# Kernel optimization log

Hardware: AMD Instinct MI355X
Metric: run time of the kernel (lower is better)

Reference implementation:

```python
import jax, jax.numpy as jnp
import numpy as np

G, N, E, F, C, H = 2, 20000, 160000, 128, 64, 8
NEG_SLOPE = 0.2


def setup_inputs() -> dict:
    key = jax.random.key(0)
    ks = jax.random.split(key, 16)
    def w(k, shape, fan_in):
        return jax.random.normal(k, shape, jnp.float32) * (1.0 / np.sqrt(fan_in))
    z = lambda *s: jnp.zeros(s, jnp.float32)
    return {
        "x": jax.random.normal(ks[0], (G, N, F), jnp.float32),
        "edge_index": jax.random.randint(ks[1], (G, 2, E), 0, N, jnp.int32),
        "edge_weight": jax.random.uniform(ks[2], (G, E), jnp.float32),
        "Wl1": w(ks[3], (F, H * C), F), "bl1": z(H * C),
        "Wr1": w(ks[4], (F, H * C), F), "br1": z(H * C),
        "We1": w(ks[5], (1, H * C), 1),
        "att1": w(ks[6], (H, C), C),
        "bias1": z(H * C),
        "Wl2": w(ks[7], (H * C, C), H * C), "bl2": z(C),
        "Wr2": w(ks[8], (H * C, C), H * C), "br2": z(C),
        "We2": w(ks[9], (1, C), 1),
        "att2": w(ks[10], (1, C), C),
        "bias2": z(C),
        "Wg": w(ks[11], (C, C), C), "bg": z(C),
        "Wn": w(ks[12], (2 * C, C), 2 * C), "bn": z(C),
        "Wo": w(ks[13], (C, 1), C), "bo": z(1),
    }


def _segment_softmax(logits, seg, n):
    m = jax.ops.segment_max(logits, seg, num_segments=n)
    ex = jnp.exp(logits - m[seg])
    den = jax.ops.segment_sum(ex, seg, num_segments=n)
    return ex / den[seg]


def _gatv2(x, src, dst, eattr, Wl, bl, Wr, br, We, att, bias, heads, concat):
    # Faithful PyG GATv2Conv (share_weights=False, edge_dim=1).
    n = x.shape[0]
    hc = Wl.shape[1]
    c = hc // heads
    xl = (x @ Wl + bl).reshape(n, heads, c)   # lin_l (source / message)
    xr = (x @ Wr + br).reshape(n, heads, c)   # lin_r (target)
    ee = (eattr @ We).reshape(-1, heads, c)   # lin_edge (bias=False)
    s = jax.nn.leaky_relu(xl[src] + xr[dst] + ee, NEG_SLOPE)  # [Etot, H, C]
    logit = jnp.einsum('ehc,hc->eh', s, att)
    alpha = _segment_softmax(logit, dst, n)   # softmax over incoming edges
    out = jax.ops.segment_sum(alpha[..., None] * xl[src], dst, num_segments=n)
    out = out.reshape(n, hc) if concat else out.mean(axis=1)
    return out + bias


def _forward(edge_index, x, edge_weight, Wl1, bl1, Wr1, br1, We1, att1, bias1,
             Wl2, bl2, Wr2, br2, We2, att2, bias2, Wg, bg, Wn, bn, Wo, bo):
    n = x.shape[1]
    def per_graph(xg, eig, ewg):
        src, dst = eig[0], eig[1]
        ea = ewg[:, None]  # edge_weight.unsqueeze(-1), edge_dim=1
        # add_self_loops with fill_value='mean' (mean of edge_attr grouped by dst)
        cnt = jax.ops.segment_sum(jnp.ones_like(ewg), dst, num_segments=n)
        loop = jax.ops.segment_sum(ea, dst, num_segments=n) / jnp.clip(cnt, 1.0)[:, None]
        ar = jnp.arange(n, dtype=src.dtype)
        src2 = jnp.concatenate([src, ar])
        dst2 = jnp.concatenate([dst, ar])
        ea2 = jnp.concatenate([ea, loop], axis=0)
        h = jax.nn.elu(_gatv2(xg, src2, dst2, ea2, Wl1, bl1, Wr1, br1, We1, att1, bias1, H, True))
        h = jax.nn.elu(_gatv2(h, src2, dst2, ea2, Wl2, bl2, Wr2, br2, We2, att2, bias2, 1, False))
        return h
    h = jax.vmap(per_graph)(x, edge_index, edge_weight)      # [G, N, C]
    g_emb = h.max(axis=1)                                    # global_max_pool per graph
    Gv = g_emb.max(axis=0)                                   # max over graphs -> [C]
    Gv = jax.nn.relu(Gv @ Wg + bg)
    Hc = jnp.concatenate([h, jnp.broadcast_to(Gv, h.shape)], axis=-1)  # [G,N,2C]
    h2 = jax.nn.relu(Hc @ Wn + bn)
    return (h2 @ Wo + bo)[..., 0]                            # [G, N] logits


def reference(x, edge_index, edge_weight, Wl1, bl1, Wr1, br1, We1, att1, bias1,
              Wl2, bl2, Wr2, br2, We2, att2, bias2, Wg, bg, Wn, bn, Wo, bo):
    return _forward(edge_index, x, edge_weight, Wl1, bl1, Wr1, br1, We1, att1, bias1,
                    Wl2, bl2, Wr2, br2, We2, att2, bias2, Wg, bg, Wn, bn, Wo, bo)
```

## Files before the change

### kernel.cpp

```cpp
#include <hip/hip_runtime.h>
#include <hip/hip_bf16.h>
#include <cstdint>
#include <cstddef>

#define NEG_SLOPE 0.2f

static constexpr int Gg = 2;
static constexpr int Nn = 20000;
static constexpr int Ee = 160000;
static constexpr int Ff = 128;
static constexpr int Cc = 64;
static constexpr int HC = 512;
static constexpr int GN = Gg * Nn;
static constexpr int GNP = 40064;

typedef __attribute__((ext_vector_type(8))) short short8;
typedef __attribute__((ext_vector_type(4))) float floatx4;

__device__ __forceinline__ float bf2f(unsigned short b) {
    return __uint_as_float(((unsigned)b) << 16);
}
__device__ __forceinline__ unsigned short f2bf(float x) {
    unsigned u = __float_as_uint(x);
    unsigned r = 0x7fffu + ((u >> 16) & 1u);
    return (unsigned short)((u + r) >> 16);
}
__device__ __forceinline__ void unpack8(const uint4 p, float* f) {
    f[0] = __uint_as_float(p.x << 16); f[1] = __uint_as_float(p.x & 0xffff0000u);
    f[2] = __uint_as_float(p.y << 16); f[3] = __uint_as_float(p.y & 0xffff0000u);
    f[4] = __uint_as_float(p.z << 16); f[5] = __uint_as_float(p.z & 0xffff0000u);
    f[6] = __uint_as_float(p.w << 16); f[7] = __uint_as_float(p.w & 0xffff0000u);
}
__device__ __forceinline__ unsigned encf(float x) {
    unsigned u = __float_as_uint(x);
    return (u & 0x80000000u) ? ~u : (u | 0x80000000u);
}
__device__ __forceinline__ float decf(unsigned e) {
    return __uint_as_float((e & 0x80000000u) ? (e ^ 0x80000000u) : ~e);
}

__global__ void zero_init_k(int* cnt, float* lsum, unsigned* gmax) {
    int idx = blockIdx.x * 256 + threadIdx.x;
    if (idx < GN) { cnt[idx] = 0; lsum[idx] = 0.f; }
    if (idx < 64) gmax[idx] = 0u;
}

__global__ void hist_k(const int* __restrict__ ei, const float* __restrict__ ew,
                       int* __restrict__ cnt, float* __restrict__ lsum) {
    int idx = blockIdx.x * 256 + threadIdx.x;
    if (idx >= Gg * Ee) return;
    int g = idx / Ee;
    int e = idx - g * Ee;
    int dst = ei[(size_t)g * 2 * Ee + Ee + e];
    float wv = ew[idx];
    atomicAdd(&cnt[g * Nn + dst], 1);
    atomicAdd(&lsum[g * Nn + dst], wv);
}

__global__ __launch_bounds__(1024) void scan_k(const int* __restrict__ cnt, const float* __restrict__ lsum,
                                               int* __restrict__ off, int* __restrict__ cur,
                                               float* __restrict__ loopw) {
    const int g = blockIdx.x;
    const int t = threadIdx.x;
    const int CH = 20;
    int base = t * CH;
    int cl[CH];
    int s = 0;
    if (base < Nn) {
#pragma unroll
        for (int q = 0; q < 5; ++q) {
            int4 v = *(const int4*)(cnt + (size_t)g * Nn + base + q * 4);
            cl[q * 4 + 0] = v.x; cl[q * 4 + 1] = v.y; cl[q * 4 + 2] = v.z; cl[q * 4 + 3] = v.w;
            s += v.x + v.y + v.z + v.w;
        }
    }
    __shared__ int sh[1024];
    sh[t] = s;
    __syncthreads();
    for (int d = 1; d < 1024; d <<= 1) {
        int v = (t >= d) ? sh[t - d] : 0;
        __syncthreads();
        sh[t] += v;
        __syncthreads();
    }
    int run = sh[t] - s;
    if (base < Nn) {
#pragma unroll
        for (int q = 0; q < 5; ++q) {
            int4 ov;
            ov.x = run; run += cl[q * 4 + 0];
            ov.y = run; run += cl[q * 4 + 1];
            ov.z = run; run += cl[q * 4 + 2];
            ov.w = run; run += cl[q * 4 + 3];
            *(int4*)(off + (size_t)g * Nn + base + q * 4) = ov;
            *(int4*)(cur + (size_t)g * Nn + base + q * 4) = ov;
            float4 lv = *(const float4*)(lsum + (size_t)g * Nn + base + q * 4);
            float4 lw;
            lw.x = lv.x / fmaxf((float)cl[q * 4 + 0], 1.f);
            lw.y = lv.y / fmaxf((float)cl[q * 4 + 1], 1.f);
            lw.z = lv.z / fmaxf((float)cl[q * 4 + 2], 1.f);
            lw.w = lv.w / fmaxf((float)cl[q * 4 + 3], 1.f);
            *(float4*)(loopw + (size_t)g * Nn + base + q * 4) = lw;
        }
    }
}

__global__ void scatter_k(const int* __restrict__ ei, const float* __restrict__ ew,
                          int* __restrict__ cur, int2* __restrict__ sedge) {
    int idx = blockIdx.x * 256 + threadIdx.x;
    if (idx >= Gg * Ee) return;
    int g = idx / Ee;
    int e = idx - g * Ee;
    int src = ei[(size_t)g * 2 * Ee + e];
    int dst = ei[(size_t)g * 2 * Ee + Ee + e];
    float wv = ew[idx];
    int pos = atomicAdd(&cur[g * Nn + dst], 1);
    int2 v; v.x = src; v.y = __float_as_int(wv);
    sedge[(size_t)g * Ee + pos] = v;
}

__global__ void castprep_k(const float* __restrict__ x, unsigned short* __restrict__ xb,
                           const float* __restrict__ Wl1, const float* __restrict__ Wr1,
                           const float* __restrict__ bl1, const float* __restrict__ br1,
                           const float* __restrict__ Wl2, const float* __restrict__ Wr2,
                           const float* __restrict__ bl2, const float* __restrict__ br2,
                           unsigned short* __restrict__ Wt1, unsigned short* __restrict__ Wt2,
                           float* __restrict__ b1cat, float* __restrict__ b2cat) {
    int t = blockIdx.x * 256 + threadIdx.x;
    size_t base = (size_t)t * 4;
    if (base < (size_t)GNP * Ff) {
        ushort4 ov;
        if (base < (size_t)GN * Ff) {
            float4 v = *(const float4*)(x + base);
            ov.x = f2bf(v.x); ov.y = f2bf(v.y); ov.z = f2bf(v.z); ov.w = f2bf(v.w);
        } else {
            ov.x = ov.y = ov.z = ov.w = 0;
        }
        *(ushort4*)(xb + base) = ov;
    }
    if (t < 1024 * 128) {
        int n = t >> 7, k = t & 127;
        float v = (n < 512) ? Wl1[(size_t)k * 512 + n] : Wr1[(size_t)k * 512 + n - 512];
        Wt1[t] = f2bf(v);
    }
    if (t < 128 * 512) {
        int n = t >> 9, k = t & 511;
        float v = (n < 64) ? Wl2[(size_t)k * 64 + n] : Wr2[(size_t)k * 64 + n - 64];
        Wt2[t] = f2bf(v);
    }
    if (t < 1024) b1cat[t] = (t < 512) ? bl1[t] : br1[t - 512];
    if (t < 128)  b2cat[t] = (t < 64) ? bl2[t] : br2[t - 64];
}

template <int K>
__global__ __launch_bounds__(256) void mfma_gemm_k(const unsigned short* __restrict__ A, int lda,
                                                   const unsigned short* __restrict__ Bt,
                                                   const float* __restrict__ bias,
                                                   unsigned short* __restrict__ Cg, int ldc,
                                                   int Mreal) {
    __shared__ unsigned short As[128 * 32];
    __shared__ unsigned short Bs[128 * 32];
    const int t = threadIdx.x;
    const int lane = t & 63;
    const int wid = t >> 6;
    const int wm = wid >> 1, wn = wid & 1;
    const int m0 = blockIdx.x * 128;
    const int n0 = blockIdx.y * 128;

    floatx4 acc[4][4] = {};

    const int jrow = t >> 2;
    const int js = t & 3;
    const int wavebase = (t & 192) * 16;

    for (int k0 = 0; k0 < K; k0 += 32) {
#pragma unroll
        for (int r = 0; r < 2; ++r) {
            int row = jrow + r * 64;
            int c = js ^ ((row >> 1) & 3);
            const unsigned short* gA = A + (size_t)(m0 + row) * lda + k0 + c * 8;
            const unsigned short* gB = Bt + (size_t)(n0 + row) * K + k0 + c * 8;
            __builtin_amdgcn_global_load_lds(
                (const __attribute__((address_space(1))) void*)gA,
                (__attribute__((address_space(3))) void*)((char*)As + r * 4096 + wavebase),
                16, 0, 0);
            __builtin_amdgcn_global_load_lds(
                (const __attribute__((address_space(1))) void*)gB,
                (__attribute__((address_space(3))) void*)((char*)Bs + r * 4096 + wavebase),
                16, 0, 0);
        }
        __syncthreads();

        const int lrow = lane & 15, lc = lane >> 4;
        short8 af[4], bf[4];
#pragma unroll
        for (int i2 = 0; i2 < 4; ++i2) {
            int rA = wm * 64 + i2 * 16 + lrow;
            int sA = lc ^ ((rA >> 1) & 3);
            af[i2] = *(const short8*)((const char*)As + (rA * 4 + sA) * 16);
        }
#pragma unroll
        for (int j2 = 0; j2 < 4; ++j2) {
            int rB = wn * 64 + j2 * 16 + lrow;
            int sB = lc ^ ((rB >> 1) & 3);
            bf[j2] = *(const short8*)((const char*)Bs + (rB * 4 + sB) * 16);
        }
#pragma unroll
        for (int i2 = 0; i2 < 4; ++i2)
#pragma unroll
            for (int j2 = 0; j2 < 4; ++j2)
                acc[i2][j2] = __builtin_amdgcn_mfma_f32_16x16x32_bf16(bf[j2], af[i2], acc[i2][j2], 0, 0, 0);
        __syncthreads();
    }

    const int mrow = m0 + wm * 64 + (lane & 15);
    const int ncol0 = n0 + wn * 64 + ((lane >> 4) << 2);
    float4 bq[4];
#pragma unroll
    for (int j2 = 0; j2 < 4; ++j2) bq[j2] = *(const float4*)(bias + ncol0 + j2 * 16);
#pragma unroll
    for (int i2 = 0; i2 < 4; ++i2) {
        int m = mrow + i2 * 16;
        if (m < Mreal) {
#pragma unroll
            for (int j2 = 0; j2 < 4; ++j2) {
                ushort4 ov;
                ov.x = f2bf(acc[i2][j2][0] + bq[j2].x);
                ov.y = f2bf(acc[i2][j2][1] + bq[j2].y);
                ov.z = f2bf(acc[i2][j2][2] + bq[j2].z);
                ov.w = f2bf(acc[i2][j2][3] + bq[j2].w);
                *(ushort4*)(Cg + (size_t)m * ldc + ncol0 + j2 * 16) = ov;
            }
        }
    }
}

__global__ __launch_bounds__(256) void agg1_k(const unsigned short* xlr,
                                              const int2* __restrict__ sedge,
                                              const int* __restrict__ off, const int* __restrict__ cnt,
                                              const float* __restrict__ loopw,
                                              const float* __restrict__ att1, const float* __restrict__ We1,
                                              const float* __restrict__ bias1,
                                              unsigned short* h1) {
    const int lane = threadIdx.x & 63;
    const int wid = (blockIdx.x << 2) + (threadIdx.x >> 6);
    if (wid >= GN) return;
    const int g = (wid >= Nn) ? 1 : 0;

    float attv[8], wev[8];
    {
        float4 a0 = *(const float4*)(att1 + lane * 8);
        float4 a1 = *(const float4*)(att1 + lane * 8 + 4);
        attv[0] = a0.x; attv[1] = a0.y; attv[2] = a0.z; attv[3] = a0.w;
        attv[4] = a1.x; attv[5] = a1.y; attv[6] = a1.z; attv[7] = a1.w;
        float4 w0 = *(const float4*)(We1 + lane * 8);
        float4 w1 = *(const float4*)(We1 + lane * 8 + 4);
        wev[0] = w0.x; wev[1] = w0.y; wev[2] = w0.z; wev[3] = w0.w;
        wev[4] = w1.x; wev[5] = w1.y; wev[6] = w1.z; wev[7] = w1.w;
    }
    float xrv[8];
    unpack8(((const uint4*)(xlr + (size_t)wid * 1024 + 512))[lane], xrv);

    float lsum, acc[8];
    {
        float lw = loopw[wid];
        float xv[8];
        unpack8(((const uint4*)(xlr + (size_t)wid * 1024))[lane], xv);
        float tp = 0.f;
#pragma unroll
        for (int j = 0; j < 8; ++j) {
            float s = xv[j] + fmaf(lw, wev[j], xrv[j]);
            s = fmaxf(s, NEG_SLOPE * s);
            tp = fmaf(s, attv[j], tp);
        }
        tp += __shfl_xor(tp, 1); tp += __shfl_xor(tp, 2); tp += __shfl_xor(tp, 4);
        float p = __expf(tp);
        lsum = p;
#pragma unroll
        for (int j = 0; j < 8; ++j) acc[j] = p * xv[j];
    }

    const int e0 = off[wid], ec = cnt[wid];
    const int2* ep = sedge + (size_t)g * Ee + e0;
    const uint4* rowb = (const uint4*)(xlr + (size_t)g * Nn * 1024) + lane;

    uint4 r0, r1; int2 s0v, s1v;
    if (ec > 0) { s0v = ep[0]; r0 = rowb[(size_t)s0v.x * 128]; }
    if (ec > 1) { s1v = ep[1]; r1 = rowb[(size_t)s1v.x * 128]; }
    int e = 0;
    while (e + 1 < ec) {
        uint4 r2, r3; int2 s2v, s3v;
        if (e + 2 < ec) { s2v = ep[e + 2]; r2 = rowb[(size_t)s2v.x * 128]; }
        if (e + 3 < ec) { s3v = ep[e + 3]; r3 = rowb[(size_t)s3v.x * 128]; }
        float xa[8], xb_[8];
        unpack8(r0, xa);
        unpack8(r1, xb_);
        float wa = __int_as_float(s0v.y), wb = __int_as_float(s1v.y);
        float ta = 0.f, tb = 0.f;
#pragma unroll
        for (int j = 0; j < 8; ++j) {
            float sa = xa[j] + fmaf(wa, wev[j], xrv[j]);
            float sb = xb_[j] + fmaf(wb, wev[j], xrv[j]);
            sa = fmaxf(sa, NEG_SLOPE * sa);
            sb = fmaxf(sb, NEG_SLOPE * sb);
            ta = fmaf(sa, attv[j], ta);
            tb = fmaf(sb, attv[j], tb);
        }
        ta += __shfl_xor(ta, 1); tb += __shfl_xor(tb, 1);
        ta += __shfl_xor(ta, 2); tb += __shfl_xor(tb, 2);
        ta += __shfl_xor(ta, 4); tb += __shfl_xor(tb, 4);
        float pa = __expf(ta), pb = __expf(tb);
        lsum += pa + pb;
#pragma unroll
        for (int j = 0; j < 8; ++j) acc[j] = fmaf(pa, xa[j], fmaf(pb, xb_[j], acc[j]));
        r0 = r2; s0v = s2v; r1 = r3; s1v = s3v;
        e += 2;
    }
    if (e < ec) {
        float xa[8];
        unpack8(r0, xa);
        float wa = __int_as_float(s0v.y);
        float ta = 0.f;
#pragma unroll
        for (int j = 0; j < 8; ++j) {
            float sa = xa[j] + fmaf(wa, wev[j], xrv[j]);
            sa = fmaxf(sa, NEG_SLOPE * sa);
            ta = fmaf(sa, attv[j], ta);
        }
        ta += __shfl_xor(ta, 1); ta += __shfl_xor(ta, 2); ta += __shfl_xor(ta, 4);
        float pa = __expf(ta);
        lsum += pa;
#pragma unroll
        for (int j = 0; j < 8; ++j) acc[j] = fmaf(pa, xa[j], acc[j]);
    }

    float inv = 1.f / lsum;
    float4 b0 = *(const float4*)(bias1 + lane * 8);
    float4 b1 = *(const float4*)(bias1 + lane * 8 + 4);
    float bvv[8] = {b0.x, b0.y, b0.z, b0.w, b1.x, b1.y, b1.z, b1.w};
    float ov[8];
#pragma unroll
    for (int j = 0; j < 8; ++j) {
        float o = fmaf(acc[j], inv, bvv[j]);
        ov[j] = o > 0.f ? o : (__expf(o) - 1.f);
    }
    uint4 pk;
    pk.x = (unsigned)f2bf(ov[0]) | ((unsigned)f2bf(ov[1]) << 16);
    pk.y = (unsigned)f2bf(ov[2]) | ((unsigned)f2bf(ov[3]) << 16);
    pk.z = (unsigned)f2bf(ov[4]) | ((unsigned)f2bf(ov[5]) << 16);
    pk.w = (unsigned)f2bf(ov[6]) | ((unsigned)f2bf(ov[7]) << 16);
    ((uint4*)(h1 + (size_t)wid * 1024))[lane] = pk;
}

__global__ __launch_bounds__(256) void agg2_k(const unsigned short* __restrict__ xlr2,
                                              const int2* __restrict__ sedge,
                                              const int* __restrict__ off, const int* __restrict__ cnt,
                                              const float* __restrict__ loopw,
                                              const float* __restrict__ att2, const float* __restrict__ We2,
                                              const float* __restrict__ bias2,
                                              float* __restrict__ hout) {
    const int lane = threadIdx.x & 63;
    const int wid = (blockIdx.x << 2) + (threadIdx.x >> 6);
    if (wid >= GN) return;
    const int g = (wid >= Nn) ? 1 : 0;

    float attv = att2[lane];
    float wev = We2[lane];
    float xrv = bf2f(xlr2[(size_t)wid * 128 + 64 + lane]);
    const unsigned short* rowb = xlr2 + (size_t)g * Nn * 128 + lane;

    float lsum, acc;
    {
        float lw = loopw[wid];
        float xv = bf2f(xlr2[(size_t)wid * 128 + lane]);
        float s = xv + fmaf(lw, wev, xrv);
        s = fmaxf(s, NEG_SLOPE * s);
        float tp = s * attv;
#pragma unroll
        for (int msk = 1; msk < 64; msk <<= 1) tp += __shfl_xor(tp, msk);
        float p = __expf(tp);
        lsum = p; acc = p * xv;
    }

    const int e0 = off[wid], ec = cnt[wid];
    const int2* ep = sedge + (size_t)g * Ee + e0;

    unsigned short r0 = 0, r1 = 0; int2 s0v, s1v;
    if (ec > 0) { s0v = ep[0]; r0 = rowb[(size_t)s0v.x * 128]; }
    if (ec > 1) { s1v = ep[1]; r1 = rowb[(size_t)s1v.x * 128]; }
    int e = 0;
    while (e + 1 < ec) {
        unsigned short r2 = 0, r3 = 0; int2 s2v, s3v;
        if (e + 2 < ec) { s2v = ep[e + 2]; r2 = rowb[(size_t)s2v.x * 128]; }
        if (e + 3 < ec) { s3v = ep[e + 3]; r3 = rowb[(size_t)s3v.x * 128]; }
        float xa = bf2f(r0), xb_ = bf2f(r1);
        float wa = __int_as_float(s0v.y), wb = __int_as_float(s1v.y);
        float sa = xa + fmaf(wa, wev, xrv);
        float sb = xb_ + fmaf(wb, wev, xrv);
        sa = fmaxf(sa, NEG_SLOPE * sa);
        sb = fmaxf(sb, NEG_SLOPE * sb);
        float ta = sa * attv, tb = sb * attv;
#pragma unroll
        for (int msk = 1; msk < 64; msk <<= 1) { ta += __shfl_xor(ta, msk); tb += __shfl_xor(tb, msk); }
        float pa = __expf(ta), pb = __expf(tb);
        lsum += pa + pb;
        acc = fmaf(pa, xa, fmaf(pb, xb_, acc));
        r0 = r2; s0v = s2v; r1 = r3; s1v = s3v;
        e += 2;
    }
    if (e < ec) {
        float xa = bf2f(r0);
        float wa = __int_as_float(s0v.y);
        float sa = xa + fmaf(wa, wev, xrv);
        sa = fmaxf(sa, NEG_SLOPE * sa);
        float ta = sa * attv;
#pragma unroll
        for (int msk = 1; msk < 64; msk <<= 1) ta += __shfl_xor(ta, msk);
        float pa = __expf(ta);
        lsum += pa;
        acc = fmaf(pa, xa, acc);
    }

    float o = acc / lsum + bias2[lane];
    o = o > 0.f ? o : (__expf(o) - 1.f);
    hout[(size_t)wid * Cc + lane] = o;
}

__global__ __launch_bounds__(256) void maxred_k(const float* __restrict__ h, unsigned* __restrict__ gmax) {
    int tid = blockIdx.x * 256 + threadIdx.x;
    float v = -3.0e38f;
    for (size_t idx = tid; idx < (size_t)GN * Cc; idx += 256 * 256) v = fmaxf(v, h[idx]);
    __shared__ float sh[256];
    sh[threadIdx.x] = v;
    __syncthreads();
    if (threadIdx.x < 64) {
        float mm = fmaxf(fmaxf(sh[threadIdx.x], sh[threadIdx.x + 64]),
                         fmaxf(sh[threadIdx.x + 128], sh[threadIdx.x + 192]));
        atomicMax(&gmax[threadIdx.x], encf(mm));
    }
}

__global__ __launch_bounds__(64) void prep_k(const unsigned* __restrict__ gmax,
                                             const float* __restrict__ Wg, const float* __restrict__ bg,
                                             const float* __restrict__ Wn, const float* __restrict__ bn,
                                             float* __restrict__ cvec) {
    __shared__ float g0[64], g1[64];
    int t = threadIdx.x;
    g0[t] = decf(gmax[t]);
    __syncthreads();
    float a = bg[t];
    for (int c = 0; c < 64; ++c) a += g0[c] * Wg[c * 64 + t];
    g1[t] = fmaxf(a, 0.f);
    __syncthreads();
    float b = bn[t];
    for (int c = 0; c < 64; ++c) b += g1[c] * Wn[(64 + c) * 64 + t];
    cvec[t] = b;
}

__global__ __launch_bounds__(256) void final_k(const float* __restrict__ h, const float* __restrict__ Wn,
                                               const float* __restrict__ cvec, const float* __restrict__ Wo,
                                               const float* __restrict__ bo, float* __restrict__ out) {
    __shared__ float wns[64 * 64];
    for (int k = threadIdx.x; k < 64 * 64; k += 256) wns[k] = Wn[k];
    __syncthreads();
    const int lane = threadIdx.x & 63;
    const int wid = (blockIdx.x << 2) + (threadIdx.x >> 6);
    if (wid >= GN) return;
    float hv = h[(size_t)wid * Cc + lane];
    float inner = 0.f;
#pragma unroll 16
    for (int c = 0; c < 64; ++c) inner += __shfl(hv, c) * wns[c * 64 + lane];
    float v = fmaxf(inner + cvec[lane], 0.f);
    float tacc = v * Wo[lane];
#pragma unroll
    for (int msk = 1; msk < 64; msk <<= 1) tacc += __shfl_xor(tacc, msk);
    if (lane == 0) out[wid] = tacc + bo[0];
}

extern "C" void kernel_launch(void* const* d_in, const int* in_sizes, int n_in,
                              void* d_out, int out_size, void* d_ws, size_t ws_size,
                              hipStream_t stream) {
    const float* x     = (const float*)d_in[0];
    const int*   ei    = (const int*)d_in[1];
    const float* ew    = (const float*)d_in[2];
    const float* Wl1   = (const float*)d_in[3];
    const float* bl1v  = (const float*)d_in[4];
    const float* Wr1   = (const float*)d_in[5];
    const float* br1v  = (const float*)d_in[6];
    const float* We1   = (const float*)d_in[7];
    const float* att1  = (const float*)d_in[8];
    const float* bias1 = (const float*)d_in[9];
    const float* Wl2   = (const float*)d_in[10];
    const float* bl2v  = (const float*)d_in[11];
    const float* Wr2   = (const float*)d_in[12];
    const float* br2v  = (const float*)d_in[13];
    const float* We2   = (const float*)d_in[14];
    const float* att2  = (const float*)d_in[15];
    const float* bias2 = (const float*)d_in[16];
    const float* Wg    = (const float*)d_in[17];
    const float* bgv   = (const float*)d_in[18];
    const float* Wn    = (const float*)d_in[19];
    const float* bnv   = (const float*)d_in[20];
    const float* Wo    = (const float*)d_in[21];
    const float* bov   = (const float*)d_in[22];
    float* out = (float*)d_out;

    char* w = (char*)d_ws;
    size_t o = 0;
    auto take = [&](size_t b) -> char* {
        char* p = w + o;
        o += (b + 255) & ~(size_t)255;
        return p;
    };
    unsigned short* xlr1 = (unsigned short*)take((size_t)GNP * 1024 * 2);
    unsigned short* xb   = (unsigned short*)take((size_t)GNP * Ff * 2);
    unsigned short* xlr2 = (unsigned short*)take((size_t)GNP * 128 * 2);
    unsigned short* Wt1  = (unsigned short*)take(1024 * 128 * 2);
    unsigned short* Wt2  = (unsigned short*)take(128 * 512 * 2);
    float* b1cat = (float*)take(1024 * 4);
    float* b2cat = (float*)take(128 * 4);
    int*    cnt   = (int*)take((size_t)GN * 4);
    float*  lsum  = (float*)take((size_t)GN * 4);
    int*    off   = (int*)take((size_t)GN * 4);
    int*    cur   = (int*)take((size_t)GN * 4);
    float*  loopw = (float*)take((size_t)GN * 4);
    int2*   sedge = (int2*)take((size_t)Gg * Ee * 8);
    unsigned* gmax = (unsigned*)take(256);
    float*  cvec  = (float*)take(256);
    unsigned short* h1 = xlr1 + 512;
    float* hbuf = (float*)xb;

    zero_init_k<<<(GN + 255) / 256, 256, 0, stream>>>(cnt, lsum, gmax);
    hist_k<<<(Gg * Ee + 255) / 256, 256, 0, stream>>>(ei, ew, cnt, lsum);
    scan_k<<<Gg, 1024, 0, stream>>>(cnt, lsum, off, cur, loopw);
    scatter_k<<<(Gg * Ee + 255) / 256, 256, 0, stream>>>(ei, ew, cur, sedge);

    castprep_k<<<((GNP * Ff / 4) + 255) / 256, 256, 0, stream>>>(
        x, xb, Wl1, Wr1, bl1v, br1v, Wl2, Wr2, bl2v, br2v, Wt1, Wt2, b1cat, b2cat);

    mfma_gemm_k<Ff><<<dim3(GNP / 128, 8), 256, 0, stream>>>(xb, Ff, Wt1, b1cat, xlr1, 1024, GN);

    agg1_k<<<GN / 4, 256, 0, stream>>>(xlr1, sedge, off, cnt, loopw, att1, We1, bias1, h1);

    mfma_gemm_k<HC><<<dim3(GNP / 128, 1), 256, 0, stream>>>(h1, 1024, Wt2, b2cat, xlr2, 128, GN);

    agg2_k<<<GN / 4, 256, 0, stream>>>(xlr2, sedge, off, cnt, loopw, att2, We2, bias2, hbuf);

    maxred_k<<<256, 256, 0, stream>>>(hbuf, gmax);
    prep_k<<<1, 64, 0, stream>>>(gmax, Wg, bgv, Wn, bnv, cvec);
    final_k<<<GN / 4, 256, 0, stream>>>(hbuf, Wn, cvec, Wo, bov, out);

    (void)in_sizes; (void)n_in; (void)out_size; (void)ws_size;
}
```

Before: 394.3 us.

## Process four nodes per wavefront in layer-2 aggregation and use shuffle-based scan

Layer-2 aggregation now assigns 16 lanes per destination node, each handling 4 channels with vectorized 8-byte loads, so one wavefront processes four nodes at once. This cuts the attention-logit reduction from six cross-lane shuffle steps to four and quarters the grid size. Lanes in a wavefront now run until the longest of the four nodes' edge lists finishes, with masking for lanes that are already done. The CSR scan kernel also swaps its shared-memory Hillis-Steele scan, which needs many barriers, for a wavefront shuffle scan plus a small cross-wave pass.

Result: faster. 378.5 us (-4.0%).

```diff
diff --git a/kernel.cpp b/kernel.cpp
--- a/kernel.cpp
+++ b/kernel.cpp
@@ -30,6 +30,10 @@
     f[2] = __uint_as_float(p.y << 16); f[3] = __uint_as_float(p.y & 0xffff0000u);
     f[4] = __uint_as_float(p.z << 16); f[5] = __uint_as_float(p.z & 0xffff0000u);
     f[6] = __uint_as_float(p.w << 16); f[7] = __uint_as_float(p.w & 0xffff0000u);
+}
+__device__ __forceinline__ void unpack4(const uint2 p, float* f) {
+    f[0] = __uint_as_float(p.x << 16); f[1] = __uint_as_float(p.x & 0xffff0000u);
+    f[2] = __uint_as_float(p.y << 16); f[3] = __uint_as_float(p.y & 0xffff0000u);
 }
 __device__ __forceinline__ unsigned encf(float x) {
     unsigned u = __float_as_uint(x);
@@ -62,6 +66,8 @@
                                                float* __restrict__ loopw) {
     const int g = blockIdx.x;
     const int t = threadIdx.x;
+    const int lane = t & 63;
+    const int wv = t >> 6;
     const int CH = 20;
     int base = t * CH;
     int cl[CH];
@@ -74,16 +80,26 @@
             s += v.x + v.y + v.z + v.w;
         }
     }
-    __shared__ int sh[1024];
-    sh[t] = s;
+    int inc = s;
+#pragma unroll
+    for (int d = 1; d < 64; d <<= 1) {
+        int tmp = __shfl_up(inc, d);
+        if (lane >= d) inc += tmp;
+    }
+    __shared__ int wsum[16];
+    if (lane == 63) wsum[wv] = inc;
     __syncthreads();
-    for (int d = 1; d < 1024; d <<= 1) {
-        int v = (t >= d) ? sh[t - d] : 0;
-        __syncthreads();
-        sh[t] += v;
-        __syncthreads();
-    }
-    int run = sh[t] - s;
+    if (t < 16) {
+        int xv = wsum[t];
+#pragma unroll
+        for (int d = 1; d < 16; d <<= 1) {
+            int tmp = __shfl_up(xv, d);
+            if (t >= d) xv += tmp;
+        }
+        wsum[t] = xv;
+    }
+    __syncthreads();
+    int run = ((wv == 0) ? 0 : wsum[wv - 1]) + inc - s;
     if (base < Nn) {
 #pragma unroll
         for (int q = 0; q < 5; ++q) {
@@ -360,70 +376,93 @@
                                               const float* __restrict__ bias2,
                                               float* __restrict__ hout) {
     const int lane = threadIdx.x & 63;
-    const int wid = (blockIdx.x << 2) + (threadIdx.x >> 6);
-    if (wid >= GN) return;
-    const int g = (wid >= Nn) ? 1 : 0;
-
-    float attv = att2[lane];
-    float wev = We2[lane];
-    float xrv = bf2f(xlr2[(size_t)wid * 128 + 64 + lane]);
-    const unsigned short* rowb = xlr2 + (size_t)g * Nn * 128 + lane;
-
-    float lsum, acc;
+    const int cs = lane & 15;
+    const int sub = lane >> 4;
+    const int w4 = (blockIdx.x << 2) + (threadIdx.x >> 6);
+    const int node = w4 * 4 + sub;
+    const int g = (node >= Nn) ? 1 : 0;
+
+    float4 av = *(const float4*)(att2 + cs * 4);
+    float4 wv4 = *(const float4*)(We2 + cs * 4);
+    float attv[4] = {av.x, av.y, av.z, av.w};
+    float wevv[4] = {wv4.x, wv4.y, wv4.z, wv4.w};
+    float xrv[4];
+    unpack4(*(const uint2*)(xlr2 + (size_t)node * 128 + 64 + cs * 4), xrv);
+    const unsigned short* rowb = xlr2 + (size_t)g * Nn * 128;
+
+    float lsum, acc[4];
     {
-        float lw = loopw[wid];
-        float xv = bf2f(xlr2[(size_t)wid * 128 + lane]);
-        float s = xv + fmaf(lw, wev, xrv);
-        s = fmaxf(s, NEG_SLOPE * s);
-        float tp = s * attv;
-#pragma unroll
-        for (int msk = 1; msk < 64; msk <<= 1) tp += __shfl_xor(tp, msk);
+        float lw = loopw[node];
+        float xv[4];
+        unpack4(*(const uint2*)(xlr2 + (size_t)node * 128 + cs * 4), xv);
+        float tp = 0.f;
+#pragma unroll
+        for (int j = 0; j < 4; ++j) {
+            float s = xv[j] + fmaf(lw, wevv[j], xrv[j]);
+            s = fmaxf(s, NEG_SLOPE * s);
+            tp = fmaf(s, attv[j], tp);
+        }
+        tp += __shfl_xor(tp, 1); tp += __shfl_xor(tp, 2);
+        tp += __shfl_xor(tp, 4); tp += __shfl_xor(tp, 8);
         float p = __expf(tp);
-        lsum = p; acc = p * xv;
-    }
-
-    const int e0 = off[wid], ec = cnt[wid];
+        lsum = p;
+#pragma unroll
+        for (int j = 0; j < 4; ++j) acc[j] = p * xv[j];
+    }
+
+    const int e0 = off[node], ec = cnt[node];
     const int2* ep = sedge + (size_t)g * Ee + e0;
 
-    unsigned short r0 = 0, r1 = 0; int2 s0v, s1v;
-    if (ec > 0) { s0v = ep[0]; r0 = rowb[(size_t)s0v.x * 128]; }
-    if (ec > 1) { s1v = ep[1]; r1 = rowb[(size_t)s1v.x * 128]; }
+    uint2 r0 = {0, 0}, r1 = {0, 0};
+    int2 s0v = {0, 0}, s1v = {0, 0};
+    if (0 < ec) { s0v = ep[0]; r0 = *(const uint2*)(rowb + (size_t)s0v.x * 128 + cs * 4); }
+    if (1 < ec) { s1v = ep[1]; r1 = *(const uint2*)(rowb + (size_t)s1v.x * 128 + cs * 4); }
     int e = 0;
-    while (e + 1 < ec) {
-        unsigned short r2 = 0, r3 = 0; int2 s2v, s3v;
-        if (e + 2 < ec) { s2v = ep[e + 2]; r2 = rowb[(size_t)s2v.x * 128]; }
-        if (e + 3 < ec) { s3v = ep[e + 3]; r3 = rowb[(size_t)s3v.x * 128]; }
-        float xa = bf2f(r0), xb_ = bf2f(r1);
+    while (__any(e < ec)) {
+        uint2 r2 = {0, 0}, r3 = {0, 0};
+        int2 s2v = {0, 0}, s3v = {0, 0};
+        if (e + 2 < ec) { s2v = ep[e + 2]; r2 = *(const uint2*)(rowb + (size_t)s2v.x * 128 + cs * 4); }
+        if (e + 3 < ec) { s3v = ep[e + 3]; r3 = *(const uint2*)(rowb + (size_t)s3v.x * 128 + cs * 4); }
+        bool v0 = (e < ec), v1 = (e + 1 < ec);
+        float xa[4], xb_[4];
+        unpack4(r0, xa);
+        unpack4(r1, xb_);
         float wa = __int_as_float(s0v.y), wb = __int_as_float(s1v.y);
-        float sa = xa + fmaf(wa, wev, xrv);
-        float sb = xb_ + fmaf(wb, wev, xrv);
-        sa = fmaxf(sa, NEG_SLOPE * sa);
-        sb = fmaxf(sb, NEG_SLOPE * sb);
-        float ta = sa * attv, tb = sb * attv;
-#pragma unroll
-        for (int msk = 1; msk < 64; msk <<= 1) { ta += __shfl_xor(ta, msk); tb += __shfl_xor(tb, msk); }
-        float pa = __expf(ta), pb = __expf(tb);
+        float ta = 0.f, tb = 0.f;
+#pragma unroll
+        for (int j = 0; j < 4; ++j) {
+            float sa = xa[j] + fmaf(wa, wevv[j], xrv[j]);
+            float sb = xb_[j] + fmaf(wb, wevv[j], xrv[j]);
+            sa = fmaxf(sa, NEG_SLOPE * sa);
+            sb = fmaxf(sb, NEG_SLOPE * sb);
+            ta = fmaf(sa, attv[j], ta);
+            tb = fmaf(sb, attv[j], tb);
+        }
+        ta += __shfl_xor(ta, 1); tb += __shfl_xor(tb, 1);
+        ta += __shfl_xor(ta, 2); tb += __shfl_xor(tb, 2);
+        ta += __shfl_xor(ta, 4); tb += __shfl_xor(tb, 4);
+        ta += __shfl_xor(ta, 8); tb += __shfl_xor(tb, 8);
+        float pa = v0 ? __expf(ta) : 0.f;
+        float pb = v1 ? __expf(tb) : 0.f;
         lsum += pa + pb;
-        acc = fmaf(pa, xa, fmaf(pb, xb_, acc));
+#pragma unroll
+        for (int j = 0; j < 4; ++j) acc[j] = fmaf(pa, xa[j], fmaf(pb, xb_[j], acc[j]));
         r0 = r2; s0v = s2v; r1 = r3; s1v = s3v;
         e += 2;
     }
-    if (e < ec) {
-        float xa = bf2f(r0);
-        float wa = __int_as_float(s0v.y);
-        float sa = xa + fmaf(wa, wev, xrv);
-        sa = fmaxf(sa, NEG_SLOPE * sa);
-        float ta = sa * attv;
-#pragma unroll
-        for (int msk = 1; msk < 64; msk <<= 1) ta += __shfl_xor(ta, msk);
-        float pa = __expf(ta);
-        lsum += pa;
-        acc = fmaf(pa, xa, acc);
-    }
-
-    float o = acc / lsum + bias2[lane];
-    o = o > 0.f ? o : (__expf(o) - 1.f);
-    hout[(size_t)wid * Cc + lane] = o;
+
+    float inv = 1.f / lsum;
+    float4 bv = *(const float4*)(bias2 + cs * 4);
+    float bvv[4] = {bv.x, bv.y, bv.z, bv.w};
+    float4 o4;
+    float ov[4];
+#pragma unroll
+    for (int j = 0; j < 4; ++j) {
+        float o = fmaf(acc[j], inv, bvv[j]);
+        ov[j] = o > 0.f ? o : (__expf(o) - 1.f);
+    }
+    o4.x = ov[0]; o4.y = ov[1]; o4.z = ov[2]; o4.w = ov[3];
+    *(float4*)(hout + (size_t)node * Cc + cs * 4) = o4;
 }
 
 __global__ __launch_bounds__(256) void maxred_k(const float* __restrict__ h, unsigned* __restrict__ gmax) {
@@ -544,7 +583,7 @@
 
     mfma_gemm_k<HC><<<dim3(GNP / 128, 1), 256, 0, stream>>>(h1, 1024, Wt2, b2cat, xlr2, 128, GN);
 
-    agg2_k<<<GN / 4, 256, 0, stream>>>(xlr2, sedge, off, cnt, loopw, att2, We2, bias2, hbuf);
+    agg2_k<<<GN / 16, 256, 0, stream>>>(xlr2, sedge, off, cnt, loopw, att2, We2, bias2, hbuf);
 
     maxred_k<<<256, 256, 0, stream>>>(hbuf, gmax);
     prep_k<<<1, 64, 0, stream>>>(gmax, Wg, bgv, Wn, bnv, cvec);
```
